# Kernel tuning notes

Hardware: AMD Instinct MI355X
Metric: run time of the kernel (lower is better)

Reference implementation:

```python
import jax, jax.numpy as jnp
import numpy as np

B, T, D, H = 4, 4096, 1280, 5120  # batch, tokens (64x64 SAM grid), embedding_dim, mlp_dim


def setup_inputs() -> dict:
    key = jax.random.key(0)
    k = jax.random.split(key, 5)
    # int8 quantized activations and weights (symmetric, per-tensor)
    x = jax.random.randint(k[0], (B, T, D), -128, 128, dtype=jnp.int8)
    w1 = jax.random.randint(k[1], (H, D), -128, 128, dtype=jnp.int8)  # lin1.weight [out,in]
    b1 = jax.random.normal(k[2], (H,), jnp.float32) * 0.02            # fp32 bias
    w2 = jax.random.randint(k[3], (D, H), -128, 128, dtype=jnp.int8)  # lin2.weight [out,in]
    b2 = jax.random.normal(k[4], (D,), jnp.float32) * 0.02
    a1 = jnp.float32(0.05 * 0.01)   # input_scale * w1_scale (dequant alpha of lin1)
    s_req = jnp.float32(0.08)       # lin2_input_scale (requant scale after GELU)
    a2 = jnp.float32(0.08 * 0.01)   # lin2_input_scale * w2_scale (dequant alpha of lin2)
    return dict(x=x, w1=w1, b1=b1, w2=w2, b2=b2, a1=a1, s_req=s_req, a2=a2)


def reference(x, w1, b1, w2, b2, a1, s_req, a2):
    acc1 = jnp.einsum('btd,hd->bth', x.astype(jnp.int32), w1.astype(jnp.int32))
    h = acc1.astype(jnp.float32) * a1 + b1              # [B,T,H] fp32
    # exact (erf) GELU, then requantize to int8 for lin2's input
    g = jax.nn.gelu(h, approximate=False)
    q = jnp.clip(jnp.round(g / s_req), -128, 127).astype(jnp.int8)
    acc2 = jnp.einsum('bth,dh->btd', q.astype(jnp.int32), w2.astype(jnp.int32))
    return acc2.astype(jnp.float32) * a2 + b2           # [B,T,D] fp32
```

## Files before the change

### kernel.cpp

```cpp
#include <hip/hip_runtime.h>
#include <stdint.h>
#include <math.h>

typedef __attribute__((ext_vector_type(4))) int i32x4;
typedef __attribute__((ext_vector_type(16))) int i32x16;
typedef __attribute__((ext_vector_type(4))) float f32x4;

constexpr int D_DIM = 1280;
constexpr int H_DIM = 5120;

__device__ __forceinline__ void gload_lds16(const void* g, void* l) {
  __builtin_amdgcn_global_load_lds(
      (const __attribute__((address_space(1))) void*)g,
      (__attribute__((address_space(3))) void*)l,
      16, 0, 0);
}

__global__ void __launch_bounds__(256) k_packw(const int* __restrict__ s1,
                                               const int* __restrict__ s2,
                                               int8_t* __restrict__ out,
                                               long wn) {
  long i = ((long)blockIdx.x * 256 + threadIdx.x) * 16;
  const int* p = (i < wn) ? (s1 + i) : (s2 + (i - wn));
  i32x4 a = *(const i32x4*)(p);
  i32x4 b = *(const i32x4*)(p + 4);
  i32x4 c = *(const i32x4*)(p + 8);
  i32x4 d = *(const i32x4*)(p + 12);
  i32x4 r;
  r.x = (a.x & 255) | ((a.y & 255) << 8) | ((a.z & 255) << 16) | (a.w << 24);
  r.y = (b.x & 255) | ((b.y & 255) << 8) | ((b.z & 255) << 16) | (b.w << 24);
  r.z = (c.x & 255) | ((c.y & 255) << 8) | ((c.z & 255) << 16) | (c.w << 24);
  r.w = (d.x & 255) | ((d.y & 255) << 8) | ((d.z & 255) << 16) | (d.w << 24);
  *(i32x4*)(out + i) = r;
}

__global__ void __launch_bounds__(256) k_pack(const int* __restrict__ in,
                                              int8_t* __restrict__ out,
                                              long n) {
  long i = ((long)blockIdx.x * 256 + threadIdx.x) * 16;
  if (i >= n) return;
  const int* p = in + i;
  i32x4 a = *(const i32x4*)(p);
  i32x4 b = *(const i32x4*)(p + 4);
  i32x4 c = *(const i32x4*)(p + 8);
  i32x4 d = *(const i32x4*)(p + 12);
  i32x4 r;
  r.x = (a.x & 255) | ((a.y & 255) << 8) | ((a.z & 255) << 16) | (a.w << 24);
  r.y = (b.x & 255) | ((b.y & 255) << 8) | ((b.z & 255) << 16) | (b.w << 24);
  r.z = (c.x & 255) | ((c.y & 255) << 8) | ((c.z & 255) << 16) | (c.w << 24);
  r.w = (d.x & 255) | ((d.y & 255) << 8) | ((d.z & 255) << 16) | (d.w << 24);
  *(i32x4*)(out + i) = r;
}

template <int KDIM, int NDIM, bool GELU>
__global__ void __launch_bounds__(256, 2)
k_gemm(const int8_t* __restrict__ A, const int8_t* __restrict__ B,
       const float* __restrict__ bias, const float* __restrict__ ps1,
       const float* __restrict__ ps2, void* __restrict__ Cout, int Mtiles) {
  constexpr int BM = 128, BN = 128, BKB = 128;
  constexpr int NT = KDIM / BKB;
  constexpr int BNC = NDIM / BN;
  constexpr int G = BNC * 4;

  __shared__ __align__(16) int8_t smem[4 * 16384];

  const int nwg = Mtiles * BNC;
  int bm, bn;
  {
    const int bid = blockIdx.x;
    const int q = nwg >> 3, r = nwg & 7, x = bid & 7, l = bid >> 3;
    const int swz = (x < r ? x * (q + 1) : r * (q + 1) + (x - r) * q) + l;
    if ((Mtiles & 3) == 0) {
      const int g = swz / G, rr = swz % G;
      bn = rr >> 2;
      bm = g * 4 + (rr & 3);
    } else {
      bn = swz % BNC;
      bm = swz / BNC;
    }
  }

  const int tid = threadIdx.x;
  const int lane = tid & 63, wid = tid >> 6;
  const int wr = wid >> 1, wc = wid & 1;

  const int srow = tid >> 3;
  const int soff = (((tid & 7) ^ (srow & 7)) << 4);
  const int8_t* Ath = A + (size_t)(bm * BM + srow) * KDIM + soff;
  const int8_t* Bth = B + (size_t)(bn * BN + srow) * KDIM + soff;
  const int dT = tid * 16;

  auto STAGE = [&](int boff, const int8_t* ga, const int8_t* gb) {
#pragma unroll
    for (int p = 0; p < 4; ++p)
      gload_lds16(ga + (size_t)(p * 32) * KDIM, smem + boff + dT + p * 4096);
#pragma unroll
    for (int p = 0; p < 4; ++p)
      gload_lds16(gb + (size_t)(p * 32) * KDIM,
                  smem + 32768 + boff + dT + p * 4096);
  };

  const int r32 = lane & 31, hi5 = lane >> 5;
  const int fsw = (lane & 7) << 4;
  const int kq = hi5 << 4;
  const int8_t* aP[4];
  const int8_t* bP[4];
#pragma unroll
  for (int ks = 0; ks < 4; ++ks) {
    const int koff = (ks * 32 + kq) ^ fsw;
    aP[ks] = smem + (wr * 64 + r32) * BKB + koff;
    bP[ks] = smem + 32768 + (wc * 64 + r32) * BKB + koff;
  }

  i32x16 acc[2][2] = {};

  auto COMPUTE = [&](int boff) {
#pragma unroll
    for (int ks = 0; ks < 4; ++ks) {
      i32x4 a0 = *(const i32x4*)(aP[ks] + boff);
      i32x4 a1 = *(const i32x4*)(aP[ks] + boff + 4096);
      i32x4 b0 = *(const i32x4*)(bP[ks] + boff);
      i32x4 b1 = *(const i32x4*)(bP[ks] + boff + 4096);
      if constexpr (GELU) {
        acc[0][0] = __builtin_amdgcn_mfma_i32_32x32x32_i8(b0, a0, acc[0][0], 0, 0, 0);
        acc[0][1] = __builtin_amdgcn_mfma_i32_32x32x32_i8(b0, a1, acc[0][1], 0, 0, 0);
        acc[1][0] = __builtin_amdgcn_mfma_i32_32x32x32_i8(b1, a0, acc[1][0], 0, 0, 0);
        acc[1][1] = __builtin_amdgcn_mfma_i32_32x32x32_i8(b1, a1, acc[1][1], 0, 0, 0);
      } else {
        acc[0][0] = __builtin_amdgcn_mfma_i32_32x32x32_i8(a0, b0, acc[0][0], 0, 0, 0);
        acc[0][1] = __builtin_amdgcn_mfma_i32_32x32x32_i8(a0, b1, acc[0][1], 0, 0, 0);
        acc[1][0] = __builtin_amdgcn_mfma_i32_32x32x32_i8(a1, b0, acc[1][0], 0, 0, 0);
        acc[1][1] = __builtin_amdgcn_mfma_i32_32x32x32_i8(a1, b1, acc[1][1], 0, 0, 0);
      }
    }
  };

  STAGE(0, Ath, Bth);
  __syncthreads();
  const int8_t* gA = Ath + BKB;
  const int8_t* gB = Bth + BKB;
#pragma unroll 1
  for (int t = 0; t < NT; t += 2) {
    STAGE(16384, gA, gB);
    COMPUTE(0);
    __syncthreads();
    if (t + 2 < NT) STAGE(0, gA + BKB, gB + BKB);
    COMPUTE(16384);
    __syncthreads();
    gA += 2 * BKB;
    gB += 2 * BKB;
  }

  if constexpr (GELU) {
    const float s1 = *ps1;
    const float rs = 1.0f / (*ps2);
    int8_t* Q = (int8_t*)Cout;
    int8_t* lb = smem;
#pragma unroll
    for (int n = 0; n < 2; ++n) {
#pragma unroll
      for (int q = 0; q < 4; ++q) {
        const int hl = wc * 64 + n * 32 + q * 8 + hi5 * 4;
        const f32x4 bv = *(const f32x4*)(bias + bn * BN + hl);
#pragma unroll
        for (int m = 0; m < 2; ++m) {
          const int tok = wr * 64 + m * 32 + r32;
          uint32_t pk = 0;
#pragma unroll
          for (int rr = 0; rr < 4; ++rr) {
            const float h = __builtin_fmaf((float)acc[n][m][q * 4 + rr], s1, bv[rr]);
            const float e = __expf(-1.702f * h);
            const float g = h * __builtin_amdgcn_rcpf(1.0f + e);
            float qf = rintf(g * rs);
            qf = fminf(127.0f, fmaxf(-128.0f, qf));
            pk |= ((uint32_t)((int)qf & 255)) << (rr * 8);
          }
          *(uint32_t*)(lb + tok * 132 + hl) = pk;
        }
      }
    }
    __syncthreads();
#pragma unroll
    for (int it = 0; it < 4; ++it) {
      const int row = it * 32 + (tid >> 3);
      const int sl = tid & 7;
      const int8_t* rp = lb + row * 132 + sl * 16;
      i32x4 v;
      v.x = *(const int*)(rp);
      v.y = *(const int*)(rp + 4);
      v.z = *(const int*)(rp + 8);
      v.w = *(const int*)(rp + 12);
      *(i32x4*)(Q + (size_t)(bm * BM + row) * NDIM + bn * BN + sl * 16) = v;
    }
  } else {
    const float s1 = *ps1;
    float* O = (float*)Cout;
    const int colb = bn * BN + wc * 64 + r32;
#pragma unroll
    for (int n = 0; n < 2; ++n) {
      const int col = colb + n * 32;
      const float bv = bias[col];
#pragma unroll
      for (int m = 0; m < 2; ++m) {
        const int rowb = bm * BM + wr * 64 + m * 32 + hi5 * 4;
#pragma unroll
        for (int q = 0; q < 4; ++q)
#pragma unroll
          for (int rr = 0; rr < 4; ++rr) {
            const int row = rowb + q * 8 + rr;
            O[(size_t)row * NDIM + col] =
                __builtin_fmaf((float)acc[m][n][q * 4 + rr], s1, bv);
          }
      }
    }
  }
}

extern "C" void kernel_launch(void* const* d_in, const int* in_sizes, int n_in,
                              void* d_out, int out_size, void* d_ws, size_t ws_size,
                              hipStream_t stream) {
  (void)in_sizes; (void)n_in; (void)out_size;
  const int*   x32  = (const int*)d_in[0];
  const int*   w132 = (const int*)d_in[1];
  const float* b1   = (const float*)d_in[2];
  const int*   w232 = (const int*)d_in[3];
  const float* b2   = (const float*)d_in[4];
  const float* a1   = (const float*)d_in[5];
  const float* sreq = (const float*)d_in[6];
  const float* a2   = (const float*)d_in[7];
  float* out = (float*)d_out;

  const int M = 4 * 4096;
  const size_t WN = (size_t)H_DIM * D_DIM;
  constexpr int BM = 128, BN = 128;

  int8_t* w1p  = (int8_t*)d_ws;
  int8_t* w2p  = w1p + WN;
  int8_t* base = w2p + WN;

  size_t avail = ws_size > 2 * WN ? ws_size - 2 * WN : 0;
  size_t rows = avail / (size_t)(D_DIM + H_DIM);
  int Mc = (int)((rows / BM) * BM);
  if (Mc > M) Mc = M;
  if (Mc < BM) Mc = BM;

  k_packw<<<(int)(2 * WN / 4096), 256, 0, stream>>>(w132, w232, w1p, (long)WN);

  for (int m0 = 0; m0 < M; m0 += Mc) {
    const int mc = (M - m0 < Mc) ? (M - m0) : Mc;
    int8_t* xp = base;
    int8_t* q  = base + (size_t)Mc * D_DIM;
    const size_t nx = (size_t)mc * D_DIM;
    const int mt = mc / BM;
    k_pack<<<(int)(nx / 4096), 256, 0, stream>>>(x32 + (size_t)m0 * D_DIM, xp, (long)nx);
    k_gemm<D_DIM, H_DIM, true><<<mt * (H_DIM / BN), 256, 0, stream>>>(
        xp, w1p, b1, a1, sreq, q, mt);
    k_gemm<H_DIM, D_DIM, false><<<mt * (D_DIM / BN), 256, 0, stream>>>(
        q, w2p, b2, a2, nullptr, out + (size_t)m0 * D_DIM, mt);
  }
}
```

Before: 284.4 us.

## Fuse weight and activation packing, raise MFMA priority, use nontemporal stores

When the workspace holds the whole batch, the weight pack and the activation pack are merged into one kernel launch, which removes a launch and its serialization. MFMA issue is wrapped in s_setprio(1)/s_setprio(0) so the wave gets scheduling priority during its matrix ops. The epilogue stores of the int8 intermediate and the fp32 output become nontemporal to reduce cache pollution. The nontemporal Q store could hurt if the second GEMM would otherwise read Q from cache.

```diff
diff --git a/kernel.cpp b/kernel.cpp
--- a/kernel.cpp
+++ b/kernel.cpp
@@ -16,12 +16,7 @@
       16, 0, 0);
 }
 
-__global__ void __launch_bounds__(256) k_packw(const int* __restrict__ s1,
-                                               const int* __restrict__ s2,
-                                               int8_t* __restrict__ out,
-                                               long wn) {
-  long i = ((long)blockIdx.x * 256 + threadIdx.x) * 16;
-  const int* p = (i < wn) ? (s1 + i) : (s2 + (i - wn));
+__device__ __forceinline__ i32x4 pack16(const int* __restrict__ p) {
   i32x4 a = *(const i32x4*)(p);
   i32x4 b = *(const i32x4*)(p + 4);
   i32x4 c = *(const i32x4*)(p + 8);
@@ -31,7 +26,19 @@
   r.y = (b.x & 255) | ((b.y & 255) << 8) | ((b.z & 255) << 16) | (b.w << 24);
   r.z = (c.x & 255) | ((c.y & 255) << 8) | ((c.z & 255) << 16) | (c.w << 24);
   r.w = (d.x & 255) | ((d.y & 255) << 8) | ((d.z & 255) << 16) | (d.w << 24);
-  *(i32x4*)(out + i) = r;
+  return r;
+}
+
+__global__ void __launch_bounds__(256) k_pack3(const int* __restrict__ s1,
+                                               const int* __restrict__ s2,
+                                               const int* __restrict__ s3,
+                                               int8_t* __restrict__ out,
+                                               long wn, long nx) {
+  long i = ((long)blockIdx.x * 256 + threadIdx.x) * 16;
+  if (i >= 2 * wn + nx) return;
+  const int* p = (i < wn) ? (s1 + i)
+               : (i < 2 * wn) ? (s2 + (i - wn)) : (s3 + (i - 2 * wn));
+  *(i32x4*)(out + i) = pack16(p);
 }
 
 __global__ void __launch_bounds__(256) k_pack(const int* __restrict__ in,
@@ -39,17 +46,7 @@
                                               long n) {
   long i = ((long)blockIdx.x * 256 + threadIdx.x) * 16;
   if (i >= n) return;
-  const int* p = in + i;
-  i32x4 a = *(const i32x4*)(p);
-  i32x4 b = *(const i32x4*)(p + 4);
-  i32x4 c = *(const i32x4*)(p + 8);
-  i32x4 d = *(const i32x4*)(p + 12);
-  i32x4 r;
-  r.x = (a.x & 255) | ((a.y & 255) << 8) | ((a.z & 255) << 16) | (a.w << 24);
-  r.y = (b.x & 255) | ((b.y & 255) << 8) | ((b.z & 255) << 16) | (b.w << 24);
-  r.z = (c.x & 255) | ((c.y & 255) << 8) | ((c.z & 255) << 16) | (c.w << 24);
-  r.w = (d.x & 255) | ((d.y & 255) << 8) | ((d.z & 255) << 16) | (d.w << 24);
-  *(i32x4*)(out + i) = r;
+  *(i32x4*)(out + i) = pack16(in + i);
 }
 
 template <int KDIM, int NDIM, bool GELU>
@@ -121,6 +118,7 @@
       i32x4 a1 = *(const i32x4*)(aP[ks] + boff + 4096);
       i32x4 b0 = *(const i32x4*)(bP[ks] + boff);
       i32x4 b1 = *(const i32x4*)(bP[ks] + boff + 4096);
+      __builtin_amdgcn_s_setprio(1);
       if constexpr (GELU) {
         acc[0][0] = __builtin_amdgcn_mfma_i32_32x32x32_i8(b0, a0, acc[0][0], 0, 0, 0);
         acc[0][1] = __builtin_amdgcn_mfma_i32_32x32x32_i8(b0, a1, acc[0][1], 0, 0, 0);
@@ -132,6 +130,7 @@
         acc[1][0] = __builtin_amdgcn_mfma_i32_32x32x32_i8(a1, b0, acc[1][0], 0, 0, 0);
         acc[1][1] = __builtin_amdgcn_mfma_i32_32x32x32_i8(a1, b1, acc[1][1], 0, 0, 0);
       }
+      __builtin_amdgcn_s_setprio(0);
     }
   };
 
@@ -190,7 +189,8 @@
       v.y = *(const int*)(rp + 4);
       v.z = *(const int*)(rp + 8);
       v.w = *(const int*)(rp + 12);
-      *(i32x4*)(Q + (size_t)(bm * BM + row) * NDIM + bn * BN + sl * 16) = v;
+      __builtin_nontemporal_store(
+          v, (i32x4*)(Q + (size_t)(bm * BM + row) * NDIM + bn * BN + sl * 16));
     }
   } else {
     const float s1 = *ps1;
@@ -208,8 +208,9 @@
 #pragma unroll
           for (int rr = 0; rr < 4; ++rr) {
             const int row = rowb + q * 8 + rr;
-            O[(size_t)row * NDIM + col] =
-                __builtin_fmaf((float)acc[m][n][q * 4 + rr], s1, bv);
+            __builtin_nontemporal_store(
+                __builtin_fmaf((float)acc[m][n][q * 4 + rr], s1, bv),
+                &O[(size_t)row * NDIM + col]);
           }
       }
     }
@@ -244,8 +245,22 @@
   if (Mc > M) Mc = M;
   if (Mc < BM) Mc = BM;
 
-  k_packw<<<(int)(2 * WN / 4096), 256, 0, stream>>>(w132, w232, w1p, (long)WN);
-
+  if (Mc == M) {
+    const long nx = (long)M * D_DIM;
+    const long tot = 2 * (long)WN + nx;
+    int8_t* xp = base;
+    int8_t* q  = base + (size_t)M * D_DIM;
+    k_pack3<<<(int)(tot / 4096), 256, 0, stream>>>(w132, w232, x32, w1p,
+                                                   (long)WN, nx);
+    k_gemm<D_DIM, H_DIM, true><<<(M / BM) * (H_DIM / BN), 256, 0, stream>>>(
+        xp, w1p, b1, a1, sreq, q, M / BM);
+    k_gemm<H_DIM, D_DIM, false><<<(M / BM) * (D_DIM / BN), 256, 0, stream>>>(
+        q, w2p, b2, a2, nullptr, out, M / BM);
+    return;
+  }
+
+  k_pack3<<<(int)(2 * WN / 4096), 256, 0, stream>>>(w132, w232, x32, w1p,
+                                                    (long)WN, 0);
   for (int m0 = 0; m0 < M; m0 += Mc) {
     const int mc = (M - m0 < Mc) ? (M - m0) : Mc;
     int8_t* xp = base;
```

After: 297.5 us. 4.6% more time.
